# Kernel optimization log

Hardware: AMD Instinct MI355X
Metric: run time of the kernel (lower is better)

Reference implementation:

```python
import jax, jax.numpy as jnp
import numpy as np

N_IN = 27          # N + 1 (alphabet + blank)
HIDDEN = 1024


def _gru(x, W_ih, W_hh, b_ih, b_hh):
    # x: [B, T, I]; weights follow PyTorch GRU layout (3H rows: r, z, n)
    gi = jnp.einsum('bti,gi->btg', x, W_ih) + b_ih  # [B, T, 3H], input GEMM hoisted out of scan

    def step(h, gi_t):
        gh = h @ W_hh.T + b_hh                      # [B, 3H]
        i_r, i_z, i_n = jnp.split(gi_t, 3, axis=-1)
        h_r, h_z, h_n = jnp.split(gh, 3, axis=-1)
        r = jax.nn.sigmoid(i_r + h_r)
        z = jax.nn.sigmoid(i_z + h_z)
        n = jnp.tanh(i_n + r * h_n)
        h_new = (1.0 - z) * n + z * h
        return h_new, h_new

    h0 = jnp.zeros((x.shape[0], W_hh.shape[1]), x.dtype)
    _, ys = jax.lax.scan(step, h0, jnp.swapaxes(gi, 0, 1))  # scan over time
    return jnp.swapaxes(ys, 0, 1)                            # [B, T, H]


def setup_inputs() -> dict:
    key = jax.random.key(0)
    ks = jax.random.split(key, 8)
    B, T = 64, 1024
    s = 1.0 / np.sqrt(HIDDEN)
    return {
        'x': jax.random.normal(ks[0], (B, T, N_IN), dtype=jnp.float32),
        'delays': jax.random.randint(ks[1], (B,), 0, 16, dtype=jnp.int64),
        'W_ih': jax.random.uniform(ks[2], (3 * HIDDEN, N_IN), jnp.float32, -s, s),
        'W_hh': jax.random.uniform(ks[3], (3 * HIDDEN, HIDDEN), jnp.float32, -s, s),
        'b_ih': jax.random.uniform(ks[4], (3 * HIDDEN,), jnp.float32, -s, s),
        'b_hh': jax.random.uniform(ks[5], (3 * HIDDEN,), jnp.float32, -s, s),
        'W_dec': jax.random.uniform(ks[6], (N_IN, HIDDEN), jnp.float32, -s, s),
        'b_dec': jax.random.uniform(ks[7], (N_IN,), jnp.float32, -s, s),
    }


def reference(x, delays, W_ih, W_hh, b_ih, b_hh, W_dec, b_dec):
    y_hat = _gru(x, W_ih, W_hh, b_ih, b_hh)          # [B, T, H]
    T = x.shape[1]
    j = jnp.arange(T)[None, :]                        # [1, T]
    d = delays[:, None]                               # [B, 1]
    idx = jnp.where(j < d, j, j - d)                  # vectorized delay gather index
    delayed = jnp.take_along_axis(y_hat, idx[:, :, None], axis=1)  # [B, T, H]
    logits = jnp.einsum('bth,oh->bto', delayed, W_dec) + b_dec
    return logits
```

## Files before the change

kernel.cpp:

```cpp
#include <hip/hip_runtime.h>

typedef short bf16x8 __attribute__((ext_vector_type(8)));
typedef float f32x4 __attribute__((ext_vector_type(4)));
typedef unsigned u32x4 __attribute__((ext_vector_type(4)));

#define T_STEPS 1024
#define NBATCH  64
#define HID     1024
#define NIN     27
#define RINGN   32
#define LAG     8
#define BPG     16
#define NWG     256

#define RINGHI_BYTES ((size_t)RINGN * NBATCH * HID * 2)
#define FLAGS_INTS   (NWG * 16)
#define FLAGS_BYTES  ((size_t)FLAGS_INTS * sizeof(int))
#define WS_NEED      (RINGHI_BYTES + FLAGS_BYTES)

__device__ __forceinline__ unsigned short f2bf(float f) {
    unsigned u = __float_as_uint(f);
    unsigned r = u + 0x7FFFu + ((u >> 16) & 1u);
    return (unsigned short)(r >> 16);
}
__device__ __forceinline__ float bf2f(unsigned short h) {
    return __uint_as_float(((unsigned)h) << 16);
}

__device__ __forceinline__ void ld_b128_sys(const void* p, u32x4& v) {
    asm volatile("global_load_dwordx4 %0, %1, off sc0 sc1" : "=v"(v) : "v"(p));
}
__device__ __forceinline__ void ld_b32_sys(const void* p, unsigned& v) {
    asm volatile("global_load_dword %0, %1, off sc0 sc1" : "=v"(v) : "v"(p));
}
__device__ __forceinline__ int ld_flag_sys(const int* p) {
    int v;
    asm volatile("global_load_dword %0, %1, off sc0 sc1\n\ts_waitcnt vmcnt(0)"
                 : "=v"(v) : "v"(p) : "memory");
    return v;
}
__device__ __forceinline__ void st_b32_sys(void* p, unsigned v) {
    asm volatile("global_store_dword %0, %1, off sc0 sc1" :: "v"(p), "v"(v) : "memory");
}
__device__ __forceinline__ void wait_vm0() {
    asm volatile("s_waitcnt vmcnt(0)" ::: "memory");
    __builtin_amdgcn_sched_barrier(0);
}

__global__ __launch_bounds__(256, 1)
void gru_persist(const float* __restrict__ x,
                 const int* __restrict__ delays,
                 const float* __restrict__ W_ih,
                 const float* __restrict__ W_hh,
                 const float* __restrict__ b_ih,
                 const float* __restrict__ b_hh,
                 const float* __restrict__ W_dec,
                 float* __restrict__ out,
                 unsigned short* __restrict__ ring_hi,
                 int* __restrict__ flags)
{
    const int tid  = threadIdx.x;
    const int lane = tid & 63;
    const int kq   = tid >> 6;
    const int gb   = blockIdx.x >> 6;
    const int gs   = blockIdx.x & 63;
    const int j0   = gs * 16;
    const int l15  = lane & 15;
    const int lhi  = lane >> 4;
    const int Bg   = gb * BPG;

    __shared__ f32x4 red[13 * 64];
    __shared__ float ylds[2][256];
    __shared__ float bias_lds[64];

    bf16x8 wHH[3][8];
    #pragma unroll
    for (int n = 0; n < 3; ++n) {
        const float* wrow = W_hh + (size_t)(n * HID + j0 + l15) * HID;
        #pragma unroll
        for (int c = 0; c < 8; ++c) {
            const float* wr = wrow + kq * 256 + c * 32 + lhi * 8;
            #pragma unroll
            for (int jj = 0; jj < 8; ++jj) wHH[n][c][jj] = (short)f2bf(wr[jj]);
        }
    }
    bf16x8 wXH[3];
    #pragma unroll
    for (int n = 0; n < 3; ++n) {
        const float* wrow = W_ih + (size_t)(n * HID + j0 + l15) * NIN;
        #pragma unroll
        for (int jj = 0; jj < 8; ++jj) {
            const int kk = lhi * 8 + jj;
            wXH[n][jj] = (kk < NIN) ? (short)f2bf(wrow[kk]) : (short)0;
        }
    }
    if (tid < 16) {
        bias_lds[tid]      = b_ih[j0 + tid] + b_hh[j0 + tid];
        bias_lds[16 + tid] = b_ih[HID + j0 + tid] + b_hh[HID + j0 + tid];
        bias_lds[32 + tid] = b_ih[2 * HID + j0 + tid];
        bias_lds[48 + tid] = b_hh[2 * HID + j0 + tid];
    }
    const int bdec  = Bg + (gs >> 2);
    const int qdec  = gs & 3;
    const int d_del = delays[bdec];
    const int odec  = tid & 31;
    const int jgd   = tid >> 5;
    float wd[32];
    #pragma unroll
    for (int jj = 0; jj < 32; ++jj)
        wd[jj] = (odec < NIN) ? W_dec[(size_t)odec * HID + qdec * 256 + jgd * 32 + jj] : 0.f;

    const int jl = l15;
    const int bl = kq * 4 + lhi;
    const int arow = Bg + l15;

    int* myflag = flags + (gb * 64 + gs) * 16;
    const int* pollflag = flags + (gb * 64 + kq * 16 + l15) * 16;

    float hprev = 0.f;
    bool dead = false;

    __syncthreads();

    #pragma clang loop unroll(disable)
    for (int t = 0; t < T_STEPS + LAG; ++t) {
        const int target = (t < T_STEPS) ? t : T_STEPS;
        const int t_dec  = t - LAG;
        const int slot_prev = (t + RINGN - 1) & (RINGN - 1);

        unsigned ydw = 0;
        if (t_dec >= 0 && tid < 128) {
            const int tau = (t_dec < d_del) ? t_dec : (t_dec - d_del);
            const unsigned* yrow = (const unsigned*)(ring_hi
                + ((size_t)((tau & (RINGN - 1)) * NBATCH + bdec)) * HID + qdec * 256);
            ld_b32_sys(yrow + tid, ydw);
        }
        bf16x8 axH = {}, axL = {};
        if (t < T_STEPS && kq == 0) {
            const float* xr = x + ((size_t)arow * T_STEPS + t) * NIN;
            #pragma unroll
            for (int jj = 0; jj < 8; ++jj) {
                const int kk = lhi * 8 + jj;
                if (kk < NIN) {
                    float f = xr[kk];
                    unsigned short hi = f2bf(f);
                    axH[jj] = (short)hi;
                    axL[jj] = (short)f2bf(f - bf2f(hi));
                }
            }
        }
        __builtin_amdgcn_sched_barrier(0);

        if (target > 0 && !dead) {
            int iter = 0;
            for (;;) {
                int v = target;
                if (lane < 16) v = ld_flag_sys(pollflag);
                if (__all(v >= target)) break;
                if (++iter > (1 << 16)) { dead = true; break; }
            }
        }
        wait_vm0();

        u32x4 rawH[8];
        if (t < T_STEPS) {
            const unsigned short* aH = ring_hi + ((size_t)(slot_prev * NBATCH + arow)) * HID
                                     + kq * 256 + lhi * 8;
            #pragma unroll
            for (int c = 0; c < 8; ++c) ld_b128_sys(aH + c * 32, rawH[c]);
        }

        f32x4 z4 = {0.f, 0.f, 0.f, 0.f};
        f32x4 acc0 = z4, acc1 = z4, acc2 = z4, acc2x = z4;

        if (t < T_STEPS) {
            if (kq == 0) {
                acc0  = __builtin_amdgcn_mfma_f32_16x16x32_bf16(axH, wXH[0], acc0, 0, 0, 0);
                acc1  = __builtin_amdgcn_mfma_f32_16x16x32_bf16(axH, wXH[1], acc1, 0, 0, 0);
                acc2x = __builtin_amdgcn_mfma_f32_16x16x32_bf16(axH, wXH[2], acc2x, 0, 0, 0);
                acc0  = __builtin_amdgcn_mfma_f32_16x16x32_bf16(axL, wXH[0], acc0, 0, 0, 0);
                acc1  = __builtin_amdgcn_mfma_f32_16x16x32_bf16(axL, wXH[1], acc1, 0, 0, 0);
                acc2x = __builtin_amdgcn_mfma_f32_16x16x32_bf16(axL, wXH[2], acc2x, 0, 0, 0);
            }
            wait_vm0();
            #pragma unroll
            for (int c = 0; c < 8; ++c) {
                bf16x8 a = __builtin_bit_cast(bf16x8, rawH[c]);
                acc0 = __builtin_amdgcn_mfma_f32_16x16x32_bf16(a, wHH[0][c], acc0, 0, 0, 0);
                acc1 = __builtin_amdgcn_mfma_f32_16x16x32_bf16(a, wHH[1][c], acc1, 0, 0, 0);
                acc2 = __builtin_amdgcn_mfma_f32_16x16x32_bf16(a, wHH[2][c], acc2, 0, 0, 0);
            }
            red[(0 * 4 + kq) * 64 + lane] = acc0;
            red[(1 * 4 + kq) * 64 + lane] = acc1;
            red[(2 * 4 + kq) * 64 + lane] = acc2;
            if (kq == 0) red[12 * 64 + lane] = acc2x;
        } else {
            wait_vm0();
        }
        if (t_dec >= 0 && tid < 128) {
            ylds[t & 1][2 * tid]     = bf2f((unsigned short)(ydw & 0xFFFFu));
            ylds[t & 1][2 * tid + 1] = bf2f((unsigned short)(ydw >> 16));
        }
        __syncthreads();

        if (t < T_STEPS) {
            const float* redf = (const float*)red;
            const int ridx = (jl + 16 * (bl >> 2)) * 4 + (bl & 3);
            float gr = 0.f, gz = 0.f, gh_n = 0.f;
            #pragma unroll
            for (int w = 0; w < 4; ++w) {
                gr   += redf[((0 * 4 + w) * 64) * 4 + ridx];
                gz   += redf[((1 * 4 + w) * 64) * 4 + ridx];
                gh_n += redf[((2 * 4 + w) * 64) * 4 + ridx];
            }
            const float i_n = redf[(12 * 64) * 4 + ridx];
            const float r  = 1.f / (1.f + __expf(-(gr + bias_lds[jl])));
            const float z  = 1.f / (1.f + __expf(-(gz + bias_lds[16 + jl])));
            const float nn = tanhf(i_n + bias_lds[32 + jl] + r * (gh_n + bias_lds[48 + jl]));
            const float hnew = (1.f - z) * nn + z * hprev;
            hprev = hnew;
            const unsigned short hih = f2bf(hnew);
            const unsigned nhi = __shfl_xor((unsigned)hih, 1);
            if ((l15 & 1) == 0) {
                const unsigned dhi = (unsigned)hih | (nhi << 16);
                const int bg = Bg + bl;
                unsigned short* ph = ring_hi
                    + ((size_t)((t & (RINGN - 1)) * NBATCH + bg)) * HID + j0 + jl;
                st_b32_sys(ph, dhi);
            }
        }
        float pdec = 0.f;
        if (t_dec >= 0) {
            if (odec < NIN) {
                const float* yrow = ylds[t & 1] + jgd * 32;
                #pragma unroll
                for (int k = 0; k < 32; ++k) pdec += yrow[k] * wd[k];
            }
            pdec += __shfl_xor(pdec, 32);
        }
        wait_vm0();
        __syncthreads();

        if (t < T_STEPS && tid == 0 && !dead)
            st_b32_sys(myflag, (unsigned)(t + 1));

        if (t < T_STEPS && tid < 16) {
            const unsigned* pf = (const unsigned*)ring_hi
                + ((size_t)((t & (RINGN - 1)) * NBATCH + Bg + tid)) * (HID / 2) + (j0 >> 1);
            unsigned dummy;
            ld_b32_sys(pf, dummy);
        }

        if (t_dec >= 0 && lane < 32 && odec < NIN)
            atomicAdd(out + ((size_t)bdec * T_STEPS + t_dec) * NIN + odec, pdec);
    }
}

__global__ void fill_out_kernel(float* __restrict__ out, const float* __restrict__ b_dec, int n)
{
    int idx = blockIdx.x * blockDim.x + threadIdx.x;
    if (idx < n) out[idx] = b_dec[idx % NIN];
}

extern "C" void kernel_launch(void* const* d_in, const int* in_sizes, int n_in,
                              void* d_out, int out_size, void* d_ws, size_t ws_size,
                              hipStream_t stream)
{
    (void)in_sizes; (void)n_in;
    const float* xx    = (const float*)d_in[0];
    const int*   dl    = (const int*)d_in[1];
    const float* W_ih  = (const float*)d_in[2];
    const float* W_hh  = (const float*)d_in[3];
    const float* b_ih  = (const float*)d_in[4];
    const float* b_hh  = (const float*)d_in[5];
    const float* W_dec = (const float*)d_in[6];
    const float* b_dec = (const float*)d_in[7];
    float* out = (float*)d_out;

    if (ws_size < WS_NEED) return;

    unsigned short* ring_hi = (unsigned short*)d_ws;
    int*            flags   = (int*)((char*)d_ws + RINGHI_BYTES);

    const size_t slot_bytes = (size_t)NBATCH * HID * 2;
    hipMemsetAsync((char*)d_ws + (size_t)(RINGN - 1) * slot_bytes, 0,
                   slot_bytes + FLAGS_BYTES, stream);

    fill_out_kernel<<<dim3((out_size + 255) / 256), dim3(256), 0, stream>>>(out, b_dec, out_size);

    void* args[] = {(void*)&xx, (void*)&dl, (void*)&W_ih, (void*)&W_hh, (void*)&b_ih,
                    (void*)&b_hh, (void*)&W_dec, (void*)&out, (void*)&ring_hi, (void*)&flags};
    hipError_t e = hipLaunchCooperativeKernel((void*)gru_persist, dim3(NWG), dim3(256),
                                              args, 0, stream);
    if (e != hipSuccess) {
        gru_persist<<<dim3(NWG), dim3(256), 0, stream>>>(xx, dl, W_ih, W_hh, b_ih, b_hh,
                                                         W_dec, out, ring_hi, flags);
    }
}
```

Baseline: 4.132 ms.

## Use full per-timestep hidden history so state loads can use normal cached loads

When the workspace is large enough, each timestep's hidden state goes to its own slot instead of a 32-entry ring. Because no slot is ever reused, the readers swap system-coherent (sc0 sc1) loads for plain cached loads, drop one vmcnt wait, and drop the cache-priming dummy load. The goal is to cut latency on the critical recurrent path. The cost is roughly 134 MB of workspace, and plain loads carry a risk of reading stale data from a non-coherent L2 across XCDs on MI355X, since the slot was never read before. The small-ring path stays as a fallback.

New measurement: 3.991 ms. 1.04x faster.

```diff
diff --git a/kernel.cpp b/kernel.cpp
--- a/kernel.cpp
+++ b/kernel.cpp
@@ -9,14 +9,16 @@
 #define HID     1024
 #define NIN     27
 #define RINGN   32
+#define NSLOT   1025
 #define LAG     8
 #define BPG     16
 #define NWG     256
 
-#define RINGHI_BYTES ((size_t)RINGN * NBATCH * HID * 2)
+#define SLOT_BYTES   ((size_t)NBATCH * HID * 2)
 #define FLAGS_INTS   (NWG * 16)
 #define FLAGS_BYTES  ((size_t)FLAGS_INTS * sizeof(int))
-#define WS_NEED      (RINGHI_BYTES + FLAGS_BYTES)
+#define WS_SMALL     ((size_t)RINGN * SLOT_BYTES + FLAGS_BYTES)
+#define WS_BIG       ((size_t)NSLOT * SLOT_BYTES + FLAGS_BYTES)
 
 __device__ __forceinline__ unsigned short f2bf(float f) {
     unsigned u = __float_as_uint(f);
@@ -47,6 +49,7 @@
     __builtin_amdgcn_sched_barrier(0);
 }
 
+template<bool BIG>
 __global__ __launch_bounds__(256, 1)
 void gru_persist(const float* __restrict__ x,
                  const int* __restrict__ delays,
@@ -126,14 +129,17 @@
     for (int t = 0; t < T_STEPS + LAG; ++t) {
         const int target = (t < T_STEPS) ? t : T_STEPS;
         const int t_dec  = t - LAG;
-        const int slot_prev = (t + RINGN - 1) & (RINGN - 1);
+        const size_t slot_prev = BIG ? (size_t)t : (size_t)((t + RINGN - 1) & (RINGN - 1));
+        const size_t slot_wr   = BIG ? (size_t)(t + 1) : (size_t)(t & (RINGN - 1));
 
         unsigned ydw = 0;
         if (t_dec >= 0 && tid < 128) {
             const int tau = (t_dec < d_del) ? t_dec : (t_dec - d_del);
+            const size_t slot_y = BIG ? (size_t)(tau + 1) : (size_t)(tau & (RINGN - 1));
             const unsigned* yrow = (const unsigned*)(ring_hi
-                + ((size_t)((tau & (RINGN - 1)) * NBATCH + bdec)) * HID + qdec * 256);
-            ld_b32_sys(yrow + tid, ydw);
+                + (slot_y * NBATCH + bdec) * HID + qdec * 256);
+            if (BIG) ydw = yrow[tid];
+            else     ld_b32_sys(yrow + tid, ydw);
         }
         bf16x8 axH = {}, axL = {};
         if (t < T_STEPS && kq == 0) {
@@ -164,10 +170,15 @@
 
         u32x4 rawH[8];
         if (t < T_STEPS) {
-            const unsigned short* aH = ring_hi + ((size_t)(slot_prev * NBATCH + arow)) * HID
+            const unsigned short* aH = ring_hi + (slot_prev * NBATCH + arow) * HID
                                      + kq * 256 + lhi * 8;
-            #pragma unroll
-            for (int c = 0; c < 8; ++c) ld_b128_sys(aH + c * 32, rawH[c]);
+            if (BIG) {
+                #pragma unroll
+                for (int c = 0; c < 8; ++c) rawH[c] = *(const u32x4*)(aH + c * 32);
+            } else {
+                #pragma unroll
+                for (int c = 0; c < 8; ++c) ld_b128_sys(aH + c * 32, rawH[c]);
+            }
         }
 
         f32x4 z4 = {0.f, 0.f, 0.f, 0.f};
@@ -182,7 +193,7 @@
                 acc1  = __builtin_amdgcn_mfma_f32_16x16x32_bf16(axL, wXH[1], acc1, 0, 0, 0);
                 acc2x = __builtin_amdgcn_mfma_f32_16x16x32_bf16(axL, wXH[2], acc2x, 0, 0, 0);
             }
-            wait_vm0();
+            if (!BIG) wait_vm0();
             #pragma unroll
             for (int c = 0; c < 8; ++c) {
                 bf16x8 a = __builtin_bit_cast(bf16x8, rawH[c]);
@@ -224,8 +235,7 @@
             if ((l15 & 1) == 0) {
                 const unsigned dhi = (unsigned)hih | (nhi << 16);
                 const int bg = Bg + bl;
-                unsigned short* ph = ring_hi
-                    + ((size_t)((t & (RINGN - 1)) * NBATCH + bg)) * HID + j0 + jl;
+                unsigned short* ph = ring_hi + (slot_wr * NBATCH + bg) * HID + j0 + jl;
                 st_b32_sys(ph, dhi);
             }
         }
@@ -243,13 +253,6 @@
 
         if (t < T_STEPS && tid == 0 && !dead)
             st_b32_sys(myflag, (unsigned)(t + 1));
-
-        if (t < T_STEPS && tid < 16) {
-            const unsigned* pf = (const unsigned*)ring_hi
-                + ((size_t)((t & (RINGN - 1)) * NBATCH + Bg + tid)) * (HID / 2) + (j0 >> 1);
-            unsigned dummy;
-            ld_b32_sys(pf, dummy);
-        }
 
         if (t_dec >= 0 && lane < 32 && odec < NIN)
             atomicAdd(out + ((size_t)bdec * T_STEPS + t_dec) * NIN + odec, pdec);
@@ -277,23 +280,34 @@
     const float* b_dec = (const float*)d_in[7];
     float* out = (float*)d_out;
 
-    if (ws_size < WS_NEED) return;
+    if (ws_size < WS_SMALL) return;
 
     unsigned short* ring_hi = (unsigned short*)d_ws;
-    int*            flags   = (int*)((char*)d_ws + RINGHI_BYTES);
-
-    const size_t slot_bytes = (size_t)NBATCH * HID * 2;
-    hipMemsetAsync((char*)d_ws + (size_t)(RINGN - 1) * slot_bytes, 0,
-                   slot_bytes + FLAGS_BYTES, stream);
+    const bool big = (ws_size >= WS_BIG);
 
     fill_out_kernel<<<dim3((out_size + 255) / 256), dim3(256), 0, stream>>>(out, b_dec, out_size);
 
-    void* args[] = {(void*)&xx, (void*)&dl, (void*)&W_ih, (void*)&W_hh, (void*)&b_ih,
-                    (void*)&b_hh, (void*)&W_dec, (void*)&out, (void*)&ring_hi, (void*)&flags};
-    hipError_t e = hipLaunchCooperativeKernel((void*)gru_persist, dim3(NWG), dim3(256),
-                                              args, 0, stream);
-    if (e != hipSuccess) {
-        gru_persist<<<dim3(NWG), dim3(256), 0, stream>>>(xx, dl, W_ih, W_hh, b_ih, b_hh,
-                                                         W_dec, out, ring_hi, flags);
-    }
-}
+    if (big) {
+        int* flags = (int*)((char*)d_ws + (size_t)NSLOT * SLOT_BYTES);
+        hipMemsetAsync(d_ws, 0, SLOT_BYTES, stream);
+        hipMemsetAsync(flags, 0, FLAGS_BYTES, stream);
+        void* args[] = {(void*)&xx, (void*)&dl, (void*)&W_ih, (void*)&W_hh, (void*)&b_ih,
+                        (void*)&b_hh, (void*)&W_dec, (void*)&out, (void*)&ring_hi, (void*)&flags};
+        hipError_t e = hipLaunchCooperativeKernel((void*)gru_persist<true>, dim3(NWG), dim3(256),
+                                                  args, 0, stream);
+        if (e != hipSuccess)
+            gru_persist<true><<<dim3(NWG), dim3(256), 0, stream>>>(
+                xx, dl, W_ih, W_hh, b_ih, b_hh, W_dec, out, ring_hi, flags);
+    } else {
+        int* flags = (int*)((char*)d_ws + (size_t)RINGN * SLOT_BYTES);
+        hipMemsetAsync((char*)d_ws + (size_t)(RINGN - 1) * SLOT_BYTES, 0,
+                       SLOT_BYTES + FLAGS_BYTES, stream);
+        void* args[] = {(void*)&xx, (void*)&dl, (void*)&W_ih, (void*)&W_hh, (void*)&b_ih,
+                        (void*)&b_hh, (void*)&W_dec, (void*)&out, (void*)&ring_hi, (void*)&flags};
+        hipError_t e = hipLaunchCooperativeKernel((void*)gru_persist<false>, dim3(NWG), dim3(256),
+                                                  args, 0, stream);
+        if (e != hipSuccess)
+            gru_persist<false><<<dim3(NWG), dim3(256), 0, stream>>>(
+                xx, dl, W_ih, W_hh, b_ih, b_hh, W_dec, out, ring_hi, flags);
+    }
+}
```
